# Kernel tuning notes

Hardware: AMD Instinct MI355X
Metric: run time of the kernel (lower is better)

## Reference

```python
import jax, jax.numpy as jnp
import numpy as np


def setup_inputs() -> dict:
    key = jax.random.key(0)
    k1, k2, k3, k4 = jax.random.split(key, 4)
    B, S, IN, OUT = 4, 2048, 4096, 11008
    input = jax.random.normal(k1, (B, S, IN), dtype=jnp.float32)
    # int8-range quantized weights, stored as int32 (symmetric, zero_point = 0)
    int8_weights = jax.random.randint(k2, (OUT, IN), -128, 128, dtype=jnp.int32)
    scales = jax.random.normal(k3, (OUT,), dtype=jnp.float32)
    bias = jax.random.normal(k4, (1, OUT), dtype=jnp.float32)
    return {"input": input, "int8_weights": int8_weights, "scales": scales, "bias": bias}


def reference(input, int8_weights, scales, bias):
    # w8_a32_forward: dequantize per-output-channel (zero_point = 0) then linear.
    # out = input @ ((q_w * s_w[:, None]).T) + bias
    # Equivalent, cheaper form: scale the GEMM output per column instead of
    # materializing a second fp32 weight copy twice.
    w = int8_weights.astype(jnp.float32)            # [OUT, IN]
    acc = jnp.einsum('bsi,oi->bso', input, w)        # [B, S, OUT]
    return acc * scales + bias                       # broadcast over [B, S, OUT]
```

## Files before the change

### kernel.cpp

```cpp
#include <hip/hip_runtime.h>
#include <hip/hip_bf16.h>
#include <stdint.h>

typedef float f32x4 __attribute__((ext_vector_type(4)));
typedef int i32x4 __attribute__((ext_vector_type(4)));

__device__ __forceinline__ void gload_lds16(const void* g, void* l) {
    __builtin_amdgcn_global_load_lds(
        (const __attribute__((address_space(1))) unsigned int*)g,
        (__attribute__((address_space(3))) unsigned int*)l,
        16, 0, 0);
}

__global__ __launch_bounds__(256) void quant_rows_kernel(
        const float* __restrict__ A, signed char* __restrict__ Aq,
        float* __restrict__ qrow, int K) {
    const long row = blockIdx.x;
    const float* a = A + row * (long)K;
    signed char* o = Aq + row * (long)K;
    const int tid = threadIdx.x;
    const int nch = K >> 2;
    float amax = 0.f;
    for (int c = tid; c < nch; c += 256) {
        f32x4 v = ((const f32x4*)a)[c];
        amax = fmaxf(amax, fmaxf(fmaxf(fabsf(v[0]), fabsf(v[1])),
                                 fmaxf(fabsf(v[2]), fabsf(v[3]))));
    }
#pragma unroll
    for (int off = 32; off; off >>= 1)
        amax = fmaxf(amax, __shfl_xor(amax, off, 64));
    __shared__ float red[4];
    if ((tid & 63) == 0) red[tid >> 6] = amax;
    __syncthreads();
    amax = fmaxf(fmaxf(red[0], red[1]), fmaxf(red[2], red[3]));
    const float s = amax > 0.f ? 127.f / amax : 0.f;
    if (tid == 0) qrow[row] = amax > 0.f ? amax / 127.f : 0.f;
    for (int c = tid; c < nch; c += 256) {
        f32x4 v = ((const f32x4*)a)[c];
        int r = 0;
#pragma unroll
        for (int i = 0; i < 4; ++i) {
            int q = (int)__builtin_rintf(v[i] * s);
            r |= (q & 0xff) << (8 * i);
        }
        ((int*)o)[c] = r;
    }
}

__global__ __launch_bounds__(256) void cvt_i32_i8_kernel(
        const int* __restrict__ in, signed char* __restrict__ out, long n) {
    long base = ((long)blockIdx.x * 256 + threadIdx.x) * 16;
    long stride = (long)gridDim.x * 256 * 16;
    for (long i = base; i < n; i += stride) {
        i32x4 pk;
#pragma unroll
        for (int c = 0; c < 4; ++c) {
            i32x4 v = *(const i32x4*)(in + i + c * 4);
            pk[c] = (v[0] & 0xff) | ((v[1] & 0xff) << 8) |
                    ((v[2] & 0xff) << 16) | ((v[3] & 0xff) << 24);
        }
        *(i32x4*)(out + i) = pk;
    }
}


__device__ __forceinline__ void stage_half(const signed char* __restrict__ G,
        long grow0, int K, int kcol0, signed char* lds_region, int tid) {
    const int row  = tid >> 2;
    const int slot = tid & 3;
    const int gcol = kcol0 + ((slot ^ ((row >> 1) & 3)) << 4);
    const int wid  = tid >> 6;
    gload_lds16(G + (grow0 + row) * (long)K + gcol,
                lds_region + wid * 1024);
}

template<int BUF, int MH>
__device__ __forceinline__ void readA(const signed char* smem, i32x4 (&fa)[4],
                                      int wr, int lane) {
    const signed char* rg = smem + BUF * 32768 + MH * 8192;
    const int fr = lane & 15, kg = lane >> 4;
#pragma unroll
    for (int ml = 0; ml < 4; ++ml) {
        const int lrow = wr * 16 + ml * 32 + fr;
        fa[ml] = *(const i32x4*)(rg + lrow * 64 + ((kg ^ ((lrow >> 1) & 3)) << 4));
    }
}

template<int BUF, int NH>
__device__ __forceinline__ void readB(const signed char* smem, i32x4 (&fb)[2],
                                      int wc, int lane) {
    const signed char* rg = smem + BUF * 32768 + 16384 + NH * 8192;
    const int fr = lane & 15, kg = lane >> 4;
#pragma unroll
    for (int nl = 0; nl < 2; ++nl) {
        const int lrow = wc * 16 + nl * 64 + fr;
        fb[nl] = *(const i32x4*)(rg + lrow * 64 + ((kg ^ ((lrow >> 1) & 3)) << 4));
    }
}

template<int MH, int NH>
__device__ __forceinline__ void mfmas(i32x4 (&acc)[8][4],
                                      const i32x4 (&fa)[4], const i32x4 (&fb)[2]) {
#pragma unroll
    for (int ml = 0; ml < 4; ++ml)
#pragma unroll
        for (int nl = 0; nl < 2; ++nl)
            acc[MH * 4 + ml][NH * 2 + nl] = __builtin_amdgcn_mfma_i32_16x16x64_i8(
                fa[ml], fb[nl], acc[MH * 4 + ml][NH * 2 + nl], 0, 0, 0);
}

#define SYNC_PRE()  { __builtin_amdgcn_s_barrier();                              \
                      asm volatile("s_waitcnt lgkmcnt(0)" ::: "memory");         \
                      __builtin_amdgcn_sched_barrier(0);                         \
                      __builtin_amdgcn_s_setprio(1); }
#define POST()      { __builtin_amdgcn_s_setprio(0); __builtin_amdgcn_s_barrier(); }
#define POST_V3()   { __builtin_amdgcn_s_setprio(0);                             \
                      asm volatile("s_waitcnt vmcnt(3)" ::: "memory");           \
                      __builtin_amdgcn_s_barrier(); }
#define POST_V0()   { __builtin_amdgcn_s_setprio(0);                             \
                      asm volatile("s_waitcnt vmcnt(0)" ::: "memory");           \
                      __builtin_amdgcn_s_barrier(); }

__global__ __launch_bounds__(512, 1) void gemm_i8_8phase(
        const signed char* __restrict__ A,
        const signed char* __restrict__ W,
        const float* __restrict__ qrow,
        const float* __restrict__ scales,
        const float* __restrict__ bias,
        float* __restrict__ C,
        int M, int N, int K) {
    extern __shared__ signed char smem[];

    const int tid  = threadIdx.x;
    const int wid  = tid >> 6;
    const int lane = tid & 63;
    const int wr = wid >> 2;
    const int wc = wid & 3;
    const int fr = lane & 15;
    const int fq = lane >> 4;

    const int nwg = gridDim.x;
    const int bid = blockIdx.x;
    const int swz = ((nwg & 7) == 0) ? ((bid & 7) * (nwg >> 3) + (bid >> 3)) : bid;
    const int tiles_n = N >> 8;
    const int tm = swz / tiles_n;
    const int tn = swz % tiles_n;
    const long arow = (long)tm * 256;
    const long brow = (long)tn * 256;

    i32x4 acc[8][4] = {};
    i32x4 fa[4], fb0[2], fb1[2];

    const int NT = K >> 6;

#define STA(kt, h) stage_half(A, arow + (h) * 128, K, (kt) * 64, \
                              smem + ((kt) & 1) * 32768 + (h) * 8192, tid)
#define STB(kt, h) stage_half(W, brow + (h) * 128, K, (kt) * 64, \
                              smem + ((kt) & 1) * 32768 + 16384 + (h) * 8192, tid)

    STA(0, 0); STB(0, 0); STA(0, 1); STB(0, 1);
    STA(1, 0); STB(1, 0); STB(1, 1);
    asm volatile("s_waitcnt vmcnt(3)" ::: "memory");
    __builtin_amdgcn_s_barrier();

    for (int i = 0; i < (NT >> 1) - 1; ++i) {
        const int b = 2 * i + 1, c = 2 * i + 2, d = 2 * i + 3;
        readA<0, 0>(smem, fa, wr, lane); readB<0, 0>(smem, fb0, wc, lane); STA(b, 1);
        SYNC_PRE(); mfmas<0, 0>(acc, fa, fb0); POST();
        readB<0, 1>(smem, fb1, wc, lane); STA(c, 0);
        SYNC_PRE(); mfmas<0, 1>(acc, fa, fb1); POST();
        readA<0, 1>(smem, fa, wr, lane); STB(c, 0);
        SYNC_PRE(); mfmas<1, 0>(acc, fa, fb0); POST();
        STB(c, 1);
        SYNC_PRE(); mfmas<1, 1>(acc, fa, fb1); POST_V3();
        readA<1, 0>(smem, fa, wr, lane); readB<1, 0>(smem, fb0, wc, lane); STA(c, 1);
        SYNC_PRE(); mfmas<0, 0>(acc, fa, fb0); POST();
        readB<1, 1>(smem, fb1, wc, lane); STA(d, 0);
        SYNC_PRE(); mfmas<0, 1>(acc, fa, fb1); POST();
        readA<1, 1>(smem, fa, wr, lane); STB(d, 0);
        SYNC_PRE(); mfmas<1, 0>(acc, fa, fb0); POST();
        STB(d, 1);
        SYNC_PRE(); mfmas<1, 1>(acc, fa, fb1); POST_V3();
    }

    readA<0, 0>(smem, fa, wr, lane); readB<0, 0>(smem, fb0, wc, lane); STA(NT - 1, 1);
    SYNC_PRE(); mfmas<0, 0>(acc, fa, fb0); POST();
    readB<0, 1>(smem, fb1, wc, lane);
    SYNC_PRE(); mfmas<0, 1>(acc, fa, fb1); POST();
    readA<0, 1>(smem, fa, wr, lane);
    SYNC_PRE(); mfmas<1, 0>(acc, fa, fb0); POST();
    SYNC_PRE(); mfmas<1, 1>(acc, fa, fb1); POST_V0();
    readA<1, 0>(smem, fa, wr, lane); readB<1, 0>(smem, fb0, wc, lane);
    SYNC_PRE(); mfmas<0, 0>(acc, fa, fb0); POST();
    readB<1, 1>(smem, fb1, wc, lane);
    SYNC_PRE(); mfmas<0, 1>(acc, fa, fb1); POST();
    readA<1, 1>(smem, fa, wr, lane);
    SYNC_PRE(); mfmas<1, 0>(acc, fa, fb0); POST();
    SYNC_PRE(); mfmas<1, 1>(acc, fa, fb1);
    __builtin_amdgcn_s_setprio(0);

#undef STA
#undef STB

    float qr[8][4];
#pragma unroll
    for (int mh = 0; mh < 2; ++mh)
#pragma unroll
        for (int ml = 0; ml < 4; ++ml) {
            const long row0 = arow + wr * 16 + mh * 128 + ml * 32 + fq * 4;
#pragma unroll
            for (int j = 0; j < 4; ++j)
                qr[mh * 4 + ml][j] = qrow[row0 + j];
        }

#pragma unroll
    for (int n = 0; n < 4; ++n) {
        const int col = tn * 256 + wc * 16 + n * 64 + fr;
        const float s = scales[col];
        const float bb = bias[col];
#pragma unroll
        for (int mh = 0; mh < 2; ++mh)
#pragma unroll
            for (int ml = 0; ml < 4; ++ml) {
                const int m = mh * 4 + ml;
                const long row0 = arow + wr * 16 + mh * 128 + ml * 32 + fq * 4;
#pragma unroll
                for (int j = 0; j < 4; ++j)
                    C[(row0 + j) * (long)N + col] =
                        (float)acc[m][n][j] * (qr[m][j] * s) + bb;
            }
    }
}

__global__ __launch_bounds__(256) void gemm_fallback_kernel(
        const float* __restrict__ A, const int* __restrict__ W,
        const float* __restrict__ scales, const float* __restrict__ bias,
        float* __restrict__ C, int M, int N, int K) {
    __shared__ float As[64][16];
    __shared__ float Ws[64][16];
    const int tiles_n = N / 64;
    const int tm = blockIdx.x / tiles_n, tn = blockIdx.x % tiles_n;
    const int tid = threadIdx.x, tx = tid & 15, ty = tid >> 4;
    float acc[4][4] = {};
    for (int k0 = 0; k0 < K; k0 += 16) {
        __syncthreads();
#pragma unroll
        for (int i = 0; i < 4; ++i) {
            const int idx = tid + i * 256;
            const int r = idx >> 4, c = idx & 15;
            As[r][c] = A[(long)(tm * 64 + r) * K + k0 + c];
            Ws[r][c] = (float)W[(long)(tn * 64 + r) * K + k0 + c];
        }
        __syncthreads();
#pragma unroll
        for (int kk = 0; kk < 16; ++kk) {
            float a[4], w[4];
#pragma unroll
            for (int r = 0; r < 4; ++r) a[r] = As[ty * 4 + r][kk];
#pragma unroll
            for (int c = 0; c < 4; ++c) w[c] = Ws[tx * 4 + c][kk];
#pragma unroll
            for (int r = 0; r < 4; ++r)
#pragma unroll
                for (int c = 0; c < 4; ++c) acc[r][c] += a[r] * w[c];
        }
    }
#pragma unroll
    for (int r = 0; r < 4; ++r)
#pragma unroll
        for (int c = 0; c < 4; ++c) {
            const int col = tn * 64 + tx * 4 + c;
            C[(long)(tm * 64 + ty * 4 + r) * N + col] = acc[r][c] * scales[col] + bias[col];
        }
}

extern "C" void kernel_launch(void* const* d_in, const int* in_sizes, int n_in,
                              void* d_out, int out_size, void* d_ws, size_t ws_size,
                              hipStream_t stream) {
    const float* A32    = (const float*)d_in[0];
    const int*   Wq     = (const int*)d_in[1];
    const float* scales = (const float*)d_in[2];
    const float* bias   = (const float*)d_in[3];
    float* C = (float*)d_out;

    const long aElems = in_sizes[0];
    const long wElems = in_sizes[1];
    const int  N = in_sizes[2];
    const int  K = (int)(wElems / N);
    const int  M = (int)(aElems / K);

    const size_t need = (size_t)aElems + (size_t)wElems + (size_t)M * 4 + 64;
    const bool div256 = (M % 256 == 0) && (N % 256 == 0) && (K % 128 == 0) && (K >= 256);

    if (ws_size >= need && div256) {
        signed char* Aq  = (signed char*)d_ws;
        signed char* Wq8 = Aq + aElems;
        float* qrow = (float*)(Wq8 + wElems);
        quant_rows_kernel<<<M, 256, 0, stream>>>(A32, Aq, qrow, K);
        cvt_i32_i8_kernel<<<2048, 256, 0, stream>>>(Wq, Wq8, wElems);
        const int nwg = (M / 256) * (N / 256);
        gemm_i8_8phase<<<nwg, 512, 65536, stream>>>(Aq, Wq8, qrow, scales, bias, C, M, N, K);
    } else {
        const int nwg = (M / 64) * (N / 64);
        gemm_fallback_kernel<<<nwg, 256, 0, stream>>>(A32, Wq, scales, bias, C, M, N, K);
    }
}
```

Baseline: 490.8 us.

## Double the int8 GEMM K-tile to 128 and use nontemporal output stores

Each pipeline stage now covers 128 K elements instead of 64. The LDS double buffer grows to 128 KB, each staging call issues two 16-byte global-to-LDS loads per thread, and the XOR swizzle widens to 8 chunks. Every phase issues two MFMAs per accumulator, so barriers and phase overhead per unit of work are halved. Output stores become nontemporal to avoid cache pollution. The costs are more fragment registers, twice the LDS footprint (which relies on the larger LDS of gfx950), and a stricter K divisibility requirement for the fast path.

```diff
diff --git a/kernel.cpp b/kernel.cpp
--- a/kernel.cpp
+++ b/kernel.cpp
@@ -66,47 +66,59 @@
 
 __device__ __forceinline__ void stage_half(const signed char* __restrict__ G,
         long grow0, int K, int kcol0, signed char* lds_region, int tid) {
-    const int row  = tid >> 2;
-    const int slot = tid & 3;
-    const int gcol = kcol0 + ((slot ^ ((row >> 1) & 3)) << 4);
-    const int wid  = tid >> 6;
-    gload_lds16(G + (grow0 + row) * (long)K + gcol,
-                lds_region + wid * 1024);
+    const int r   = tid >> 3;
+    const int c8  = tid & 7;
+    const int wid = tid >> 6;
+#pragma unroll
+    for (int j = 0; j < 2; ++j) {
+        const int lrow = j * 64 + r;
+        const int gcol = kcol0 + ((c8 ^ (lrow & 7)) << 4);
+        gload_lds16(G + (grow0 + lrow) * (long)K + gcol,
+                    lds_region + j * 8192 + wid * 1024);
+    }
 }
 
 template<int BUF, int MH>
-__device__ __forceinline__ void readA(const signed char* smem, i32x4 (&fa)[4],
+__device__ __forceinline__ void readA(const signed char* smem, i32x4 (&fa)[4][2],
                                       int wr, int lane) {
-    const signed char* rg = smem + BUF * 32768 + MH * 8192;
+    const signed char* rg = smem + BUF * 65536 + MH * 16384;
     const int fr = lane & 15, kg = lane >> 4;
 #pragma unroll
     for (int ml = 0; ml < 4; ++ml) {
         const int lrow = wr * 16 + ml * 32 + fr;
-        fa[ml] = *(const i32x4*)(rg + lrow * 64 + ((kg ^ ((lrow >> 1) & 3)) << 4));
+#pragma unroll
+        for (int ks = 0; ks < 2; ++ks)
+            fa[ml][ks] = *(const i32x4*)(rg + lrow * 128 +
+                             (((ks * 4 + kg) ^ (lrow & 7)) << 4));
     }
 }
 
 template<int BUF, int NH>
-__device__ __forceinline__ void readB(const signed char* smem, i32x4 (&fb)[2],
+__device__ __forceinline__ void readB(const signed char* smem, i32x4 (&fb)[2][2],
                                       int wc, int lane) {
-    const signed char* rg = smem + BUF * 32768 + 16384 + NH * 8192;
+    const signed char* rg = smem + BUF * 65536 + 32768 + NH * 16384;
     const int fr = lane & 15, kg = lane >> 4;
 #pragma unroll
     for (int nl = 0; nl < 2; ++nl) {
         const int lrow = wc * 16 + nl * 64 + fr;
-        fb[nl] = *(const i32x4*)(rg + lrow * 64 + ((kg ^ ((lrow >> 1) & 3)) << 4));
+#pragma unroll
+        for (int ks = 0; ks < 2; ++ks)
+            fb[nl][ks] = *(const i32x4*)(rg + lrow * 128 +
+                             (((ks * 4 + kg) ^ (lrow & 7)) << 4));
     }
 }
 
 template<int MH, int NH>
 __device__ __forceinline__ void mfmas(i32x4 (&acc)[8][4],
-                                      const i32x4 (&fa)[4], const i32x4 (&fb)[2]) {
+                                      const i32x4 (&fa)[4][2], const i32x4 (&fb)[2][2]) {
 #pragma unroll
     for (int ml = 0; ml < 4; ++ml)
 #pragma unroll
         for (int nl = 0; nl < 2; ++nl)
-            acc[MH * 4 + ml][NH * 2 + nl] = __builtin_amdgcn_mfma_i32_16x16x64_i8(
-                fa[ml], fb[nl], acc[MH * 4 + ml][NH * 2 + nl], 0, 0, 0);
+#pragma unroll
+            for (int ks = 0; ks < 2; ++ks)
+                acc[MH * 4 + ml][NH * 2 + nl] = __builtin_amdgcn_mfma_i32_16x16x64_i8(
+                    fa[ml][ks], fb[nl][ks], acc[MH * 4 + ml][NH * 2 + nl], 0, 0, 0);
 }
 
 #define SYNC_PRE()  { __builtin_amdgcn_s_barrier();                              \
@@ -114,8 +126,8 @@
                       __builtin_amdgcn_sched_barrier(0);                         \
                       __builtin_amdgcn_s_setprio(1); }
 #define POST()      { __builtin_amdgcn_s_setprio(0); __builtin_amdgcn_s_barrier(); }
-#define POST_V3()   { __builtin_amdgcn_s_setprio(0);                             \
-                      asm volatile("s_waitcnt vmcnt(3)" ::: "memory");           \
+#define POST_V6()   { __builtin_amdgcn_s_setprio(0);                             \
+                      asm volatile("s_waitcnt vmcnt(6)" ::: "memory");           \
                       __builtin_amdgcn_s_barrier(); }
 #define POST_V0()   { __builtin_amdgcn_s_setprio(0);                             \
                       asm volatile("s_waitcnt vmcnt(0)" ::: "memory");           \
@@ -149,18 +161,18 @@
     const long brow = (long)tn * 256;
 
     i32x4 acc[8][4] = {};
-    i32x4 fa[4], fb0[2], fb1[2];
-
-    const int NT = K >> 6;
-
-#define STA(kt, h) stage_half(A, arow + (h) * 128, K, (kt) * 64, \
-                              smem + ((kt) & 1) * 32768 + (h) * 8192, tid)
-#define STB(kt, h) stage_half(W, brow + (h) * 128, K, (kt) * 64, \
-                              smem + ((kt) & 1) * 32768 + 16384 + (h) * 8192, tid)
+    i32x4 fa[4][2], fb0[2][2], fb1[2][2];
+
+    const int NT = K >> 7;
+
+#define STA(kt, h) stage_half(A, arow + (h) * 128, K, (kt) * 128, \
+                              smem + ((kt) & 1) * 65536 + (h) * 16384, tid)
+#define STB(kt, h) stage_half(W, brow + (h) * 128, K, (kt) * 128, \
+                              smem + ((kt) & 1) * 65536 + 32768 + (h) * 16384, tid)
 
     STA(0, 0); STB(0, 0); STA(0, 1); STB(0, 1);
     STA(1, 0); STB(1, 0); STB(1, 1);
-    asm volatile("s_waitcnt vmcnt(3)" ::: "memory");
+    asm volatile("s_waitcnt vmcnt(6)" ::: "memory");
     __builtin_amdgcn_s_barrier();
 
     for (int i = 0; i < (NT >> 1) - 1; ++i) {
@@ -172,7 +184,7 @@
         readA<0, 1>(smem, fa, wr, lane); STB(c, 0);
         SYNC_PRE(); mfmas<1, 0>(acc, fa, fb0); POST();
         STB(c, 1);
-        SYNC_PRE(); mfmas<1, 1>(acc, fa, fb1); POST_V3();
+        SYNC_PRE(); mfmas<1, 1>(acc, fa, fb1); POST_V6();
         readA<1, 0>(smem, fa, wr, lane); readB<1, 0>(smem, fb0, wc, lane); STA(c, 1);
         SYNC_PRE(); mfmas<0, 0>(acc, fa, fb0); POST();
         readB<1, 1>(smem, fb1, wc, lane); STA(d, 0);
@@ -180,7 +192,7 @@
         readA<1, 1>(smem, fa, wr, lane); STB(d, 0);
         SYNC_PRE(); mfmas<1, 0>(acc, fa, fb0); POST();
         STB(d, 1);
-        SYNC_PRE(); mfmas<1, 1>(acc, fa, fb1); POST_V3();
+        SYNC_PRE(); mfmas<1, 1>(acc, fa, fb1); POST_V6();
     }
 
     readA<0, 0>(smem, fa, wr, lane); readB<0, 0>(smem, fb0, wc, lane); STA(NT - 1, 1);
@@ -226,8 +238,9 @@
                 const long row0 = arow + wr * 16 + mh * 128 + ml * 32 + fq * 4;
 #pragma unroll
                 for (int j = 0; j < 4; ++j)
-                    C[(row0 + j) * (long)N + col] =
-                        (float)acc[m][n][j] * (qr[m][j] * s) + bb;
+                    __builtin_nontemporal_store(
+                        (float)acc[m][n][j] * (qr[m][j] * s) + bb,
+                        &C[(row0 + j) * (long)N + col]);
             }
     }
 }
@@ -290,7 +303,7 @@
     const int  M = (int)(aElems / K);
 
     const size_t need = (size_t)aElems + (size_t)wElems + (size_t)M * 4 + 64;
-    const bool div256 = (M % 256 == 0) && (N % 256 == 0) && (K % 128 == 0) && (K >= 256);
+    const bool div256 = (M % 256 == 0) && (N % 256 == 0) && (K % 256 == 0) && (K >= 512);
 
     if (ws_size >= need && div256) {
         signed char* Aq  = (signed char*)d_ws;
@@ -299,7 +312,7 @@
         quant_rows_kernel<<<M, 256, 0, stream>>>(A32, Aq, qrow, K);
         cvt_i32_i8_kernel<<<2048, 256, 0, stream>>>(Wq, Wq8, wElems);
         const int nwg = (M / 256) * (N / 256);
-        gemm_i8_8phase<<<nwg, 512, 65536, stream>>>(Aq, Wq8, qrow, scales, bias, C, M, N, K);
+        gemm_i8_8phase<<<nwg, 512, 131072, stream>>>(Aq, Wq8, qrow, scales, bias, C, M, N, K);
     } else {
         const int nwg = (M / 64) * (N / 64);
         gemm_fallback_kernel<<<nwg, 256, 0, stream>>>(A32, Wq, scales, bias, C, M, N, K);
```

New measurement: 464.0 us. 5.5% less time.

## Prefetch LDS fragments one phase ahead and precompute 32-bit staging offsets

Applied to the files above, without the earlier changes.

Restructures the 8-phase int8 MFMA main loop so LDS fragment reads for the next phase are issued after the current MFMA batch instead of before it. The A fragments are now double-buffered in registers (faA/faB) so reads can overlap compute. The vmcnt waits move to mid-phase with a lower count, and the combined barrier macros are split apart. LDS read offsets and global staging addresses are precomputed once as 32-bit ints, with a host guard that keeps M*K and N*K small enough for int indexing. This raises register pressure and reorders the waits, which may expose hazards between the async LDS fills and the fragment reads.

```diff
diff --git a/kernel.cpp b/kernel.cpp
--- a/kernel.cpp
+++ b/kernel.cpp
@@ -5,7 +5,7 @@
 typedef float f32x4 __attribute__((ext_vector_type(4)));
 typedef int i32x4 __attribute__((ext_vector_type(4)));
 
-__device__ __forceinline__ void gload_lds16(const void* g, void* l) {
+__device__ __forceinline__ void gload_lds16(const signed char* g, signed char* l) {
     __builtin_amdgcn_global_load_lds(
         (const __attribute__((address_space(1))) unsigned int*)g,
         (__attribute__((address_space(3))) unsigned int*)l,
@@ -64,38 +64,22 @@
 }
 
 
-__device__ __forceinline__ void stage_half(const signed char* __restrict__ G,
-        long grow0, int K, int kcol0, signed char* lds_region, int tid) {
-    const int row  = tid >> 2;
-    const int slot = tid & 3;
-    const int gcol = kcol0 + ((slot ^ ((row >> 1) & 3)) << 4);
-    const int wid  = tid >> 6;
-    gload_lds16(G + (grow0 + row) * (long)K + gcol,
-                lds_region + wid * 1024);
-}
-
 template<int BUF, int MH>
-__device__ __forceinline__ void readA(const signed char* smem, i32x4 (&fa)[4],
-                                      int wr, int lane) {
+__device__ __forceinline__ void readAf(const signed char* smem, i32x4 (&fa)[4],
+                                       const int (&off)[4]) {
     const signed char* rg = smem + BUF * 32768 + MH * 8192;
-    const int fr = lane & 15, kg = lane >> 4;
-#pragma unroll
-    for (int ml = 0; ml < 4; ++ml) {
-        const int lrow = wr * 16 + ml * 32 + fr;
-        fa[ml] = *(const i32x4*)(rg + lrow * 64 + ((kg ^ ((lrow >> 1) & 3)) << 4));
-    }
+#pragma unroll
+    for (int ml = 0; ml < 4; ++ml)
+        fa[ml] = *(const i32x4*)(rg + off[ml]);
 }
 
 template<int BUF, int NH>
-__device__ __forceinline__ void readB(const signed char* smem, i32x4 (&fb)[2],
-                                      int wc, int lane) {
+__device__ __forceinline__ void readBf(const signed char* smem, i32x4 (&fb)[2],
+                                       const int (&off)[2]) {
     const signed char* rg = smem + BUF * 32768 + 16384 + NH * 8192;
-    const int fr = lane & 15, kg = lane >> 4;
-#pragma unroll
-    for (int nl = 0; nl < 2; ++nl) {
-        const int lrow = wc * 16 + nl * 64 + fr;
-        fb[nl] = *(const i32x4*)(rg + lrow * 64 + ((kg ^ ((lrow >> 1) & 3)) << 4));
-    }
+#pragma unroll
+    for (int nl = 0; nl < 2; ++nl)
+        fb[nl] = *(const i32x4*)(rg + off[nl]);
 }
 
 template<int MH, int NH>
@@ -109,17 +93,13 @@
                 fa[ml], fb[nl], acc[MH * 4 + ml][NH * 2 + nl], 0, 0, 0);
 }
 
-#define SYNC_PRE()  { __builtin_amdgcn_s_barrier();                              \
-                      asm volatile("s_waitcnt lgkmcnt(0)" ::: "memory");         \
-                      __builtin_amdgcn_sched_barrier(0);                         \
-                      __builtin_amdgcn_s_setprio(1); }
-#define POST()      { __builtin_amdgcn_s_setprio(0); __builtin_amdgcn_s_barrier(); }
-#define POST_V3()   { __builtin_amdgcn_s_setprio(0);                             \
-                      asm volatile("s_waitcnt vmcnt(3)" ::: "memory");           \
-                      __builtin_amdgcn_s_barrier(); }
-#define POST_V0()   { __builtin_amdgcn_s_setprio(0);                             \
-                      asm volatile("s_waitcnt vmcnt(0)" ::: "memory");           \
-                      __builtin_amdgcn_s_barrier(); }
+#define BARw()  __builtin_amdgcn_s_barrier()
+#define LG0()   { asm volatile("s_waitcnt lgkmcnt(0)" ::: "memory"); \
+                  __builtin_amdgcn_sched_barrier(0); }
+#define P1()    __builtin_amdgcn_s_setprio(1)
+#define P0()    __builtin_amdgcn_s_setprio(0)
+#define VM2()   asm volatile("s_waitcnt vmcnt(2)" ::: "memory")
+#define VM0()   asm volatile("s_waitcnt vmcnt(0)" ::: "memory")
 
 __global__ __launch_bounds__(512, 1) void gemm_i8_8phase(
         const signed char* __restrict__ A,
@@ -132,12 +112,13 @@
     extern __shared__ signed char smem[];
 
     const int tid  = threadIdx.x;
+    const int lane = tid & 63;
     const int wid  = tid >> 6;
-    const int lane = tid & 63;
     const int wr = wid >> 2;
     const int wc = wid & 3;
     const int fr = lane & 15;
     const int fq = lane >> 4;
+    const int kg = lane >> 4;
 
     const int nwg = gridDim.x;
     const int bid = blockIdx.x;
@@ -145,59 +126,82 @@
     const int tiles_n = N >> 8;
     const int tm = swz / tiles_n;
     const int tn = swz % tiles_n;
-    const long arow = (long)tm * 256;
-    const long brow = (long)tn * 256;
+    const int arow = tm << 8;
+    const int brow = tn << 8;
+
+    int aRd[4], bRd[2];
+#pragma unroll
+    for (int ml = 0; ml < 4; ++ml) {
+        const int lrow = wr * 16 + ml * 32 + fr;
+        aRd[ml] = lrow * 64 + ((kg ^ ((lrow >> 1) & 3)) << 4);
+    }
+#pragma unroll
+    for (int nl = 0; nl < 2; ++nl) {
+        const int lrow = wc * 16 + nl * 64 + fr;
+        bRd[nl] = lrow * 64 + ((kg ^ ((lrow >> 1) & 3)) << 4);
+    }
+
+    const int srow = tid >> 2;
+    const int sswz = (((tid & 3) ^ ((srow >> 1) & 3)) << 4);
+    int aOff[2], wOff[2];
+#pragma unroll
+    for (int h = 0; h < 2; ++h) {
+        aOff[h] = (arow + h * 128 + srow) * K + sswz;
+        wOff[h] = (brow + h * 128 + srow) * K + sswz;
+    }
+    const int ldsSt = wid * 1024;
+
+#define STA(kt, h) gload_lds16(A + aOff[h] + (kt) * 64, \
+                               smem + ((kt) & 1) * 32768 + (h) * 8192 + ldsSt)
+#define STB(kt, h) gload_lds16(W + wOff[h] + (kt) * 64, \
+                               smem + ((kt) & 1) * 32768 + 16384 + (h) * 8192 + ldsSt)
 
     i32x4 acc[8][4] = {};
-    i32x4 fa[4], fb0[2], fb1[2];
+    i32x4 faA[4], faB[4], fb0[2], fb1[2];
 
     const int NT = K >> 6;
-
-#define STA(kt, h) stage_half(A, arow + (h) * 128, K, (kt) * 64, \
-                              smem + ((kt) & 1) * 32768 + (h) * 8192, tid)
-#define STB(kt, h) stage_half(W, brow + (h) * 128, K, (kt) * 64, \
-                              smem + ((kt) & 1) * 32768 + 16384 + (h) * 8192, tid)
 
     STA(0, 0); STB(0, 0); STA(0, 1); STB(0, 1);
     STA(1, 0); STB(1, 0); STB(1, 1);
     asm volatile("s_waitcnt vmcnt(3)" ::: "memory");
-    __builtin_amdgcn_s_barrier();
+    BARw();
+    readAf<0, 0>(smem, faA, aRd);
+    readBf<0, 0>(smem, fb0, bRd);
 
     for (int i = 0; i < (NT >> 1) - 1; ++i) {
         const int b = 2 * i + 1, c = 2 * i + 2, d = 2 * i + 3;
-        readA<0, 0>(smem, fa, wr, lane); readB<0, 0>(smem, fb0, wc, lane); STA(b, 1);
-        SYNC_PRE(); mfmas<0, 0>(acc, fa, fb0); POST();
-        readB<0, 1>(smem, fb1, wc, lane); STA(c, 0);
-        SYNC_PRE(); mfmas<0, 1>(acc, fa, fb1); POST();
-        readA<0, 1>(smem, fa, wr, lane); STB(c, 0);
-        SYNC_PRE(); mfmas<1, 0>(acc, fa, fb0); POST();
-        STB(c, 1);
-        SYNC_PRE(); mfmas<1, 1>(acc, fa, fb1); POST_V3();
-        readA<1, 0>(smem, fa, wr, lane); readB<1, 0>(smem, fb0, wc, lane); STA(c, 1);
-        SYNC_PRE(); mfmas<0, 0>(acc, fa, fb0); POST();
-        readB<1, 1>(smem, fb1, wc, lane); STA(d, 0);
-        SYNC_PRE(); mfmas<0, 1>(acc, fa, fb1); POST();
-        readA<1, 1>(smem, fa, wr, lane); STB(d, 0);
-        SYNC_PRE(); mfmas<1, 0>(acc, fa, fb0); POST();
-        STB(d, 1);
-        SYNC_PRE(); mfmas<1, 1>(acc, fa, fb1); POST_V3();
-    }
-
-    readA<0, 0>(smem, fa, wr, lane); readB<0, 0>(smem, fb0, wc, lane); STA(NT - 1, 1);
-    SYNC_PRE(); mfmas<0, 0>(acc, fa, fb0); POST();
-    readB<0, 1>(smem, fb1, wc, lane);
-    SYNC_PRE(); mfmas<0, 1>(acc, fa, fb1); POST();
-    readA<0, 1>(smem, fa, wr, lane);
-    SYNC_PRE(); mfmas<1, 0>(acc, fa, fb0); POST();
-    SYNC_PRE(); mfmas<1, 1>(acc, fa, fb1); POST_V0();
-    readA<1, 0>(smem, fa, wr, lane); readB<1, 0>(smem, fb0, wc, lane);
-    SYNC_PRE(); mfmas<0, 0>(acc, fa, fb0); POST();
-    readB<1, 1>(smem, fb1, wc, lane);
-    SYNC_PRE(); mfmas<0, 1>(acc, fa, fb1); POST();
-    readA<1, 1>(smem, fa, wr, lane);
-    SYNC_PRE(); mfmas<1, 0>(acc, fa, fb0); POST();
-    SYNC_PRE(); mfmas<1, 1>(acc, fa, fb1);
-    __builtin_amdgcn_s_setprio(0);
+        BARw(); LG0(); P1(); mfmas<0, 0>(acc, faA, fb0); P0();
+        readBf<0, 1>(smem, fb1, bRd); STA(b, 1);
+        BARw(); LG0(); P1(); mfmas<0, 1>(acc, faA, fb1); P0();
+        readAf<0, 1>(smem, faB, aRd); STA(c, 0);
+        BARw(); LG0(); P1(); mfmas<1, 0>(acc, faB, fb0); P0();
+        STB(c, 0); VM2();
+        BARw(); P1(); mfmas<1, 1>(acc, faB, fb1); P0();
+        readAf<1, 0>(smem, faA, aRd); readBf<1, 0>(smem, fb0, bRd); STB(c, 1);
+        BARw(); LG0(); P1(); mfmas<0, 0>(acc, faA, fb0); P0();
+        readBf<1, 1>(smem, fb1, bRd); STA(c, 1);
+        BARw(); LG0(); P1(); mfmas<0, 1>(acc, faA, fb1); P0();
+        readAf<1, 1>(smem, faB, aRd); STA(d, 0);
+        BARw(); LG0(); P1(); mfmas<1, 0>(acc, faB, fb0); P0();
+        STB(d, 0); VM2();
+        BARw(); P1(); mfmas<1, 1>(acc, faB, fb1); P0();
+        readAf<0, 0>(smem, faA, aRd); readBf<0, 0>(smem, fb0, bRd); STB(d, 1);
+    }
+
+    BARw(); LG0(); P1(); mfmas<0, 0>(acc, faA, fb0); P0();
+    readBf<0, 1>(smem, fb1, bRd); STA(NT - 1, 1);
+    BARw(); LG0(); P1(); mfmas<0, 1>(acc, faA, fb1); P0();
+    readAf<0, 1>(smem, faB, aRd);
+    BARw(); LG0(); P1(); mfmas<1, 0>(acc, faB, fb0); P0();
+    VM0();
+    BARw(); P1(); mfmas<1, 1>(acc, faB, fb1); P0();
+    readAf<1, 0>(smem, faA, aRd); readBf<1, 0>(smem, fb0, bRd);
+    BARw(); LG0(); P1(); mfmas<0, 0>(acc, faA, fb0); P0();
+    readBf<1, 1>(smem, fb1, bRd);
+    BARw(); LG0(); P1(); mfmas<0, 1>(acc, faA, fb1); P0();
+    readAf<1, 1>(smem, faB, aRd);
+    BARw(); LG0(); P1(); mfmas<1, 0>(acc, faB, fb0); P0();
+    BARw(); P1(); mfmas<1, 1>(acc, faB, fb1); P0();
 
 #undef STA
 #undef STB
@@ -207,7 +211,7 @@
     for (int mh = 0; mh < 2; ++mh)
 #pragma unroll
         for (int ml = 0; ml < 4; ++ml) {
-            const long row0 = arow + wr * 16 + mh * 128 + ml * 32 + fq * 4;
+            const int row0 = arow + wr * 16 + mh * 128 + ml * 32 + fq * 4;
 #pragma unroll
             for (int j = 0; j < 4; ++j)
                 qr[mh * 4 + ml][j] = qrow[row0 + j];
@@ -223,10 +227,10 @@
 #pragma unroll
             for (int ml = 0; ml < 4; ++ml) {
                 const int m = mh * 4 + ml;
-                const long row0 = arow + wr * 16 + mh * 128 + ml * 32 + fq * 4;
+                const int row0 = arow + wr * 16 + mh * 128 + ml * 32 + fq * 4;
 #pragma unroll
                 for (int j = 0; j < 4; ++j)
-                    C[(row0 + j) * (long)N + col] =
+                    C[(long)(row0 + j) * N + col] =
                         (float)acc[m][n][j] * (qr[m][j] * s) + bb;
             }
     }
@@ -290,7 +294,8 @@
     const int  M = (int)(aElems / K);
 
     const size_t need = (size_t)aElems + (size_t)wElems + (size_t)M * 4 + 64;
-    const bool div256 = (M % 256 == 0) && (N % 256 == 0) && (K % 128 == 0) && (K >= 256);
+    const bool div256 = (M % 256 == 0) && (N % 256 == 0) && (K % 128 == 0) && (K >= 256) &&
+                        ((long)M * K < 2000000000L) && ((long)N * K < 2000000000L);
 
     if (ws_size >= need && div256) {
         signed char* Aq  = (signed char*)d_ws;
```

Result: no change. 482.8 us (-1.6%).
